# Optimization experiments

Measured on AMD Instinct MI355X. Metric: run time of the kernel, lower is better.

Reference implementation:

```python
import jax, jax.numpy as jnp
import numpy as np

K = 1024          # num_embeddings
D = 64            # embedding_dim
EPS = 0.05        # entropic regularization epsilon
DUAL_STEPS = 10
DUAL_LR = 0.5
TEMP = 0.5        # hist_temperature
OT_W = 1.0
CC = 0.25         # commitment cost


def _norm_prob(p):
    p = jnp.clip(p, 1e-12)
    return p / p.sum()


def _dual_obj(phi, src_w, tgt_w, cost):
    src_w = _norm_prob(src_w)
    tgt_w = _norm_prob(tgt_w)
    log_tgt = jnp.log(jnp.clip(tgt_w, 1e-12))[None, :]          # [1, K]
    lse = jax.scipy.special.logsumexp(log_tgt + (-cost + phi[None, :]) / EPS, axis=1)  # [K]
    return jnp.sum(src_w * (-EPS * lse)) + jnp.sum(tgt_w * phi)


def _dual_ot_loss(src_w, tgt_w, cost):
    src_d = jax.lax.stop_gradient(src_w)
    tgt_d = jax.lax.stop_gradient(tgt_w)
    cost_d = jax.lax.stop_gradient(cost)
    grad_phi = jax.grad(_dual_obj)
    def body(_, phi):
        return phi + DUAL_LR * grad_phi(phi, src_d, tgt_d, cost_d)
    phi = jax.lax.fori_loop(0, DUAL_STEPS, body, jnp.zeros_like(tgt_d))
    return _dual_obj(jax.lax.stop_gradient(phi), src_w, tgt_w, cost)


def _gaussian_target():
    idx = jnp.arange(K, dtype=jnp.float32)
    mean = (K - 1) / 2.0
    std = K / 6.0
    t = jnp.exp(-0.5 * ((idx - mean) / std) ** 2)
    return t / jnp.clip(t.sum(), 1e-12)


def _forward(inputs, codebook):
    B, C, H, W = inputs.shape
    x_bhwc = jnp.transpose(inputs, (0, 2, 3, 1))                 # [B,H,W,C]
    flat = x_bhwc.reshape(-1, C)                                  # [N, D]
    # squared-distance matrix [N, K]
    d = (jnp.sum(flat * flat, axis=1, keepdims=True)
         + jnp.sum(codebook * codebook, axis=1)
         - 2.0 * flat @ codebook.T)
    idx = jnp.argmin(d, axis=1)                                   # [N]
    enc = jax.nn.one_hot(idx, K, dtype=jnp.float32)               # [N, K]
    # power normalize (one-hot power = sqrt(1/K) < 1, so a no-op, but faithful)
    power = jnp.sqrt(jnp.mean(enc * enc))
    enc = jnp.where(power > 1.0, enc / power, enc)
    clean_q = enc @ codebook                                      # [N, D]
    noisy_q = clean_q                                             # channel=None -> zero noise
    # training losses
    hard_hist = jnp.mean(enc, axis=0)                             # [K]
    soft = jax.nn.softmax(-d / TEMP, axis=1)                      # [N, K]
    soft_hist = jnp.mean(soft, axis=0)
    # value = hard_hist, gradient flows via soft_hist (straight-through hist)
    cw = _norm_prob(hard_hist + soft_hist - jax.lax.stop_gradient(soft_hist))
    target = _gaussian_target()
    support = jnp.arange(K, dtype=jnp.float32)
    cost = jnp.abs(support[:, None] - support[None, :])           # cdist(p=2) on 1-d support
    ot_loss = OT_W * _dual_ot_loss(cw, target, cost)
    codebook_loss = jnp.mean((clean_q - jax.lax.stop_gradient(flat)) ** 2)
    commit_loss = jnp.mean((jax.lax.stop_gradient(clean_q) - flat) ** 2)
    loss = codebook_loss + CC * commit_loss + ot_loss
    # straight-through quantized output
    nq = noisy_q.reshape(B, H, W, C)
    quantized = x_bhwc + jax.lax.stop_gradient(nq - x_bhwc)
    quantized = jnp.transpose(quantized, (0, 3, 1, 2))            # [B,C,H,W]
    avg = jnp.mean(enc, axis=0)
    perplexity = jnp.exp(-jnp.sum(avg * jnp.log(avg + 1e-10)))
    return quantized, loss, perplexity


def setup_inputs() -> dict:
    key = jax.random.key(0)
    k1, k2 = jax.random.split(key)
    inputs = jax.random.normal(k1, (32, D, 32, 32), dtype=jnp.float32)
    codebook = jax.random.uniform(k2, (K, D), minval=-1.0 / K, maxval=1.0 / K, dtype=jnp.float32)
    return {"inputs": inputs, "codebook": codebook}


def reference(inputs, codebook):
    return _forward(inputs, codebook)
```

## Files before the change

kernel.cpp:

```cpp
#include <hip/hip_runtime.h>
#include <math.h>

#define NPTS 32768
#define KCB  1024
#define DIM  64
#define HW   1024
#define CHW  65536

typedef short  bf16x8 __attribute__((ext_vector_type(8)));
typedef float  f32x16 __attribute__((ext_vector_type(16)));

__device__ __forceinline__ unsigned short f2b_rne(float f) {
  unsigned u = __float_as_uint(f);
  unsigned r = 0x7FFFu + ((u >> 16) & 1u);
  return (unsigned short)((u + r) >> 16);
}

__device__ __forceinline__ float block_sum(float v, float* scratch) {
  #pragma unroll
  for (int o = 32; o > 0; o >>= 1) v += __shfl_down(v, o, 64);
  int wid  = threadIdx.x >> 6;
  int lane = threadIdx.x & 63;
  __syncthreads();
  if (lane == 0) scratch[wid] = v;
  __syncthreads();
  float s = 0.f;
  int nw = blockDim.x >> 6;
  for (int w = 0; w < nw; ++w) s += scratch[w];
  return s;
}

__global__ __launch_bounds__(64) void k_cvt(const float* __restrict__ cb,
                                            float4* __restrict__ cbf,
                                            float* __restrict__ cnorm,
                                            int* __restrict__ hist,
                                            int* __restrict__ done2) {
  int c = blockIdx.x * 64 + threadIdx.x;
  hist[c] = 0;
  if (c == 0) *done2 = 0;
  const float4* row4 = (const float4*)(cb + c * DIM);
  float4 r[16];
  #pragma unroll
  for (int i = 0; i < 16; ++i) r[i] = row4[i];
  float s = 0.f;
  #pragma unroll
  for (int i = 0; i < 16; ++i) {
    s = fmaf(r[i].x, r[i].x, s); s = fmaf(r[i].y, r[i].y, s);
    s = fmaf(r[i].z, r[i].z, s); s = fmaf(r[i].w, r[i].w, s);
  }
  cnorm[c] = s;
  int ch = c >> 6, nt = (c >> 5) & 1, n = c & 31;
  int base = ch * 512 + nt * 256 + n;
  #pragma unroll
  for (int o = 0; o < 8; ++o) {
    float f[8] = {r[2*o].x, r[2*o].y, r[2*o].z, r[2*o].w,
                  r[2*o+1].x, r[2*o+1].y, r[2*o+1].z, r[2*o+1].w};
    unsigned hu[4];
    #pragma unroll
    for (int j = 0; j < 4; ++j) {
      unsigned short h0 = f2b_rne(f[2*j]), h1 = f2b_rne(f[2*j+1]);
      hu[j] = (unsigned)h0 | ((unsigned)h1 << 16);
    }
    int pos = base + (o >> 1) * 64 + (o & 1) * 32;
    uint4 hv = {hu[0], hu[1], hu[2], hu[3]};
    cbf[pos] = *(float4*)&hv;
  }
}

__global__ __launch_bounds__(256, 2) void k_dist(const float* __restrict__ x,
                                                 const float* __restrict__ cb,
                                                 const float4* __restrict__ cbf,
                                                 const float* __restrict__ cnorm,
                                                 int* __restrict__ hist,
                                                 float* __restrict__ msep,
                                                 int* __restrict__ done2,
                                                 float* __restrict__ out) {
  __shared__ __align__(16) union SM {
    struct {
      unsigned short lph[64][72];
      float cn[KCB];
    } g;
    struct {
      float lt[KCB + 8]; float src[KCB + 8]; float phi[KCB + 8]; float lse[KCB + 8];
    } o;
  } sm;
  __shared__ float s_sx[64], s_part[4][64];
  __shared__ unsigned long long s_pk[64][2];
  __shared__ int   s_bd[64];
  __shared__ float scratch[4];
  __shared__ int   s_flag;

  int tid = threadIdx.x;
  int t   = blockIdx.x;
  int n0  = t * 64;
  int b   = n0 >> 10;
  int hw0 = n0 & 1023;

  *(float4*)&sm.g.cn[tid * 4] = *(const float4*)(cnorm + tid * 4);

  float fx[16];
  {
    int p = tid & 63, q4 = tid >> 6;
    const float* xb = x + b * CHW + hw0 + p;
    float s = 0.f;
    unsigned short hb[16];
    #pragma unroll
    for (int i = 0; i < 16; ++i) {
      int c = q4 * 16 + i;
      float f = xb[c * HW];
      fx[i] = f;
      s = fmaf(f, f, s);
      hb[i] = f2b_rne(f);
    }
    s_part[q4][p] = s;
    #pragma unroll
    for (int j = 0; j < 8; ++j)
      *(unsigned*)&sm.g.lph[p][q4 * 16 + 2 * j] =
          (unsigned)hb[2*j] | ((unsigned)hb[2*j+1] << 16);
  }
  __syncthreads();
  if (tid < 64)
    s_sx[tid] = ((s_part[0][tid] + s_part[1][tid]) + s_part[2][tid]) + s_part[3][tid];
  __syncthreads();

  int w = tid >> 6, l = tid & 63;
  int wm = w >> 1, wn = w & 1;
  int u = l >> 5, n = l & 31;

  bf16x8 ah[4];
  {
    int pt = wm * 32 + n;
    #pragma unroll
    for (int s = 0; s < 4; ++s)
      ah[s] = *(const bf16x8*)&sm.g.lph[pt][(2 * s + u) * 8];
  }
  float sxr[16];
  #pragma unroll
  for (int r = 0; r < 16; ++r)
    sxr[r] = s_sx[wm * 32 + (r & 3) + 8 * (r >> 2) + 4 * u];

  float best[16]; int bidx[16];
  #pragma unroll
  for (int r = 0; r < 16; ++r) { best[r] = 3.4e38f; bidx[r] = 0; }

  int bofs = wn * 256 + u * 32 + n;
  const bf16x8* gb = (const bf16x8*)cbf;

  bf16x8 cbh[4], nbh[4];
  #pragma unroll
  for (int s = 0; s < 4; ++s) cbh[s] = gb[bofs + s * 64];

  #pragma unroll
  for (int ch = 0; ch < 16; ++ch) {
    if (ch < 15) {
      const bf16x8* gn = gb + (ch + 1) * 512;
      #pragma unroll
      for (int s = 0; s < 4; ++s) nbh[s] = gn[bofs + s * 64];
    }
    f32x16 acc;
    #pragma unroll
    for (int r = 0; r < 16; ++r) acc[r] = 0.f;
    #pragma unroll
    for (int s = 0; s < 4; ++s)
      acc = __builtin_amdgcn_mfma_f32_32x32x16_bf16(ah[s], cbh[s], acc, 0, 0, 0);
    int   kk  = ch * 64 + wn * 32 + n;
    float cnv = sm.g.cn[kk];
    #pragma unroll
    for (int r = 0; r < 16; ++r) {
      float dist = (sxr[r] + cnv) - 2.0f * acc[r];
      if (dist < best[r]) { best[r] = dist; bidx[r] = kk; }
    }
    if (ch < 15) {
      #pragma unroll
      for (int s = 0; s < 4; ++s) cbh[s] = nbh[s];
    }
  }

  #pragma unroll
  for (int r = 0; r < 16; ++r) {
    unsigned long long p =
        ((unsigned long long)__float_as_uint(best[r]) << 32) | (unsigned)bidx[r];
    #pragma unroll
    for (int m = 1; m < 32; m <<= 1) {
      unsigned long long o = __shfl_xor(p, m, 64);
      p = (o < p) ? o : p;
    }
    if (n == 0)
      s_pk[wm * 32 + (r & 3) + 8 * (r >> 2) + 4 * u][wn] = p;
  }
  __syncthreads();
  if (tid < 64) {
    unsigned long long a = s_pk[tid][0], c2 = s_pk[tid][1];
    unsigned long long mn = (c2 < a) ? c2 : a;
    int bd = (int)(mn & 0xffffffffull);
    s_bd[tid] = bd;
    atomicAdd(&hist[bd], 1);
  }
  __syncthreads();

  float se = 0.f;
  {
    int p = tid & 63, cg2 = tid >> 6;
    int bd = s_bd[p];
    const float* crow = cb + bd * DIM;
    float* ob = out + b * CHW + hw0 + p;
    #pragma unroll 4
    for (int i = 0; i < 16; ++i) {
      int c = cg2 * 16 + i;
      float xv   = fx[i];
      float diff = crow[c] - xv;
      se += diff * diff;
      ob[c * HW] = xv + diff;
    }
  }
  float tot = block_sum(se, scratch);
  if (tid == 0) msep[t] = tot;

  __syncthreads();
  if (tid == 0) { __threadfence(); s_flag = atomicAdd(done2, 1); }
  __syncthreads();
  if (s_flag != 511) return;
  __threadfence();

  {
    int i0  = tid * 4;
    int sl0 = i0 + 4;

    float mse_a = __hip_atomic_load(&msep[tid],       __ATOMIC_RELAXED, __HIP_MEMORY_SCOPE_AGENT);
    float mse_b = __hip_atomic_load(&msep[tid + 256], __ATOMIC_RELAXED, __HIP_MEMORY_SCOPE_AGENT);
    float msetot = block_sum(mse_a + mse_b, scratch);

    int hi[4];
    #pragma unroll
    for (int j = 0; j < 4; ++j)
      hi[j] = __hip_atomic_load(&hist[i0 + j], __ATOMIC_RELAXED,
                                __HIP_MEMORY_SCOPE_AGENT);
    float tj[4], hj[4];
    #pragma unroll
    for (int j = 0; j < 4; ++j) {
      float fi = (float)(i0 + j);
      float zz = (fi - 511.5f) / (1024.0f / 6.0f);
      tj[j] = expf(-0.5f * zz * zz);
      hj[j] = (float)hi[j] * (1.0f / 32768.0f);
    }
    float St = block_sum(tj[0] + tj[1] + tj[2] + tj[3], scratch);
    float tgt[4], ltw[4];
    float l2 = 0.f;
    #pragma unroll
    for (int j = 0; j < 4; ++j) { tgt[j] = fmaxf(tj[j] / fmaxf(St, 1e-12f), 1e-12f); l2 += tgt[j]; }
    float St2 = block_sum(l2, scratch);
    #pragma unroll
    for (int j = 0; j < 4; ++j) { tgt[j] = tgt[j] / St2; ltw[j] = logf(fmaxf(tgt[j], 1e-12f)); }

    float m1[4], srcw[4];
    float l3 = 0.f;
    #pragma unroll
    for (int j = 0; j < 4; ++j) { m1[j] = fmaxf(hj[j], 1e-12f); l3 += m1[j]; }
    float S1 = block_sum(l3, scratch);
    float l4 = 0.f;
    #pragma unroll
    for (int j = 0; j < 4; ++j) { srcw[j] = fmaxf(m1[j] / S1, 1e-12f); l4 += srcw[j]; }
    float S2 = block_sum(l4, scratch);
    float l5 = 0.f;
    #pragma unroll
    for (int j = 0; j < 4; ++j) { srcw[j] = srcw[j] / S2; l5 += hj[j] * logf(hj[j] + 1e-10f); }
    float ent = block_sum(l5, scratch);

    *(float4*)&sm.o.lt[sl0]  = *(float4*)ltw;
    *(float4*)&sm.o.src[sl0] = *(float4*)srcw;
    *(float4*)&sm.o.phi[sl0] = make_float4(0.f, 0.f, 0.f, 0.f);
    *(float4*)&sm.o.lse[sl0] = make_float4(0.f, 0.f, 0.f, 0.f);
    if (tid == 0) {
      #pragma unroll
      for (int p = 0; p < 4; ++p) {
        sm.o.lt[p] = -100.f; sm.o.src[p] = 0.f; sm.o.phi[p] = 0.f; sm.o.lse[p] = 0.f;
        sm.o.lt[KCB+4+p] = -100.f; sm.o.src[KCB+4+p] = 0.f;
        sm.o.phi[KCB+4+p] = 0.f;   sm.o.lse[KCB+4+p] = 0.f;
      }
    }
    __syncthreads();

    float ws[12];
    #pragma unroll
    for (int m = 0; m < 3; ++m) *(float4*)&ws[m*4] = *(float4*)&sm.o.src[i0 + m*4];

    float phi[4] = {0.f, 0.f, 0.f, 0.f};
    float lse[4];
    for (int it = 0; it <= 10; ++it) {
      float wl[12], wp[12];
      #pragma unroll
      for (int m = 0; m < 3; ++m) {
        *(float4*)&wl[m*4] = *(float4*)&sm.o.lt[i0 + m*4];
        *(float4*)&wp[m*4] = *(float4*)&sm.o.phi[i0 + m*4];
      }
      #pragma unroll
      for (int j = 0; j < 4; ++j) {
        float mx = -3.0e38f;
        float vv[5];
        #pragma unroll
        for (int qq = 0; qq < 5; ++qq) {
          int m = j + qq + 2;
          float a = wl[m] + (wp[m] - fabsf((float)(qq - 2))) * 20.0f;
          vv[qq] = a;
          mx = fmaxf(mx, a);
        }
        float ssum = 0.f;
        #pragma unroll
        for (int qq = 0; qq < 5; ++qq) ssum += expf(vv[qq] - mx);
        lse[j] = mx + logf(ssum);
      }
      *(float4*)&sm.o.lse[sl0] = *(float4*)lse;
      __syncthreads();
      if (it == 10) break;

      float we[12];
      #pragma unroll
      for (int m = 0; m < 3; ++m) *(float4*)&we[m*4] = *(float4*)&sm.o.lse[i0 + m*4];
      #pragma unroll
      for (int j = 0; j < 4; ++j) {
        float basej = ltw[j] + phi[j] * 20.0f;
        float cs = 0.f;
        #pragma unroll
        for (int qq = 0; qq < 5; ++qq) {
          int m = j + qq + 2;
          float a = basej - fabsf((float)(qq - 2)) * 20.0f;
          cs += ws[m] * expf(a - we[m]);
        }
        phi[j] += 0.5f * (tgt[j] - cs);
      }
      *(float4*)&sm.o.phi[sl0] = *(float4*)phi;
      __syncthreads();
    }

    float lo = 0.f;
    #pragma unroll
    for (int j = 0; j < 4; ++j) lo += srcw[j] * (-0.05f * lse[j]) + tgt[j] * phi[j];
    float ot = block_sum(lo, scratch);

    if (tid == 0) {
      out[2097152] = 1.25f * (msetot * (1.0f / 2097152.0f)) + ot;
      out[2097153] = expf(-ent);
    }
  }
}

extern "C" void kernel_launch(void* const* d_in, const int* in_sizes, int n_in,
                              void* d_out, int out_size, void* d_ws, size_t ws_size,
                              hipStream_t stream) {
  const float* x  = (const float*)d_in[0];
  const float* cb = (const float*)d_in[1];
  float* out = (float*)d_out;

  float4* cbf  = (float4*)d_ws;
  float*  cnorm = (float*)((char*)d_ws + 131072);
  int*    hist  = (int*)((char*)d_ws + 135168);
  float*  msep  = (float*)((char*)d_ws + 139264);
  int*    done2 = (int*)((char*)d_ws + 141312);

  k_cvt<<<16, 64, 0, stream>>>(cb, cbf, cnorm, hist, done2);
  k_dist<<<512, 256, 0, stream>>>(x, cb, cbf, cnorm, hist, msep, done2, out);
}
```

Baseline: 118.0 us.

## Double block size and split codebook chunks across two wave halves

Launches k_dist with 512 threads per block instead of 256. Each half of the block scans half of the codebook chunks, and the partial argmins are merged through a wider shared array. Per-thread channel loads and stores are halved, and the final OT tail is gated to the first 256 threads. The aim is more waves in flight per point tile to hide latency on the codebook loads and MFMA work. In exchange it adds a larger cross-wave reduction and raises register and occupancy pressure under the new launch bounds.

```diff
diff --git a/kernel.cpp b/kernel.cpp
--- a/kernel.cpp
+++ b/kernel.cpp
@@ -67,7 +67,7 @@
   }
 }
 
-__global__ __launch_bounds__(256, 2) void k_dist(const float* __restrict__ x,
+__global__ __launch_bounds__(512, 2) void k_dist(const float* __restrict__ x,
                                                  const float* __restrict__ cb,
                                                  const float4* __restrict__ cbf,
                                                  const float* __restrict__ cnorm,
@@ -84,10 +84,10 @@
       float lt[KCB + 8]; float src[KCB + 8]; float phi[KCB + 8]; float lse[KCB + 8];
     } o;
   } sm;
-  __shared__ float s_sx[64], s_part[4][64];
-  __shared__ unsigned long long s_pk[64][2];
+  __shared__ float s_sx[64], s_part[8][64];
+  __shared__ unsigned long long s_pk[64][4];
   __shared__ int   s_bd[64];
-  __shared__ float scratch[4];
+  __shared__ float scratch[8];
   __shared__ int   s_flag;
 
   int tid = threadIdx.x;
@@ -96,35 +96,39 @@
   int b   = n0 >> 10;
   int hw0 = n0 & 1023;
 
-  *(float4*)&sm.g.cn[tid * 4] = *(const float4*)(cnorm + tid * 4);
-
-  float fx[16];
-  {
-    int p = tid & 63, q4 = tid >> 6;
+  *(float2*)&sm.g.cn[tid * 2] = *(const float2*)(cnorm + tid * 2);
+
+  float fx[8];
+  {
+    int p = tid & 63, q8 = tid >> 6;
     const float* xb = x + b * CHW + hw0 + p;
     float s = 0.f;
-    unsigned short hb[16];
-    #pragma unroll
-    for (int i = 0; i < 16; ++i) {
-      int c = q4 * 16 + i;
+    unsigned short hb[8];
+    #pragma unroll
+    for (int i = 0; i < 8; ++i) {
+      int c = q8 * 8 + i;
       float f = xb[c * HW];
       fx[i] = f;
       s = fmaf(f, f, s);
       hb[i] = f2b_rne(f);
     }
-    s_part[q4][p] = s;
-    #pragma unroll
-    for (int j = 0; j < 8; ++j)
-      *(unsigned*)&sm.g.lph[p][q4 * 16 + 2 * j] =
+    s_part[q8][p] = s;
+    #pragma unroll
+    for (int j = 0; j < 4; ++j)
+      *(unsigned*)&sm.g.lph[p][q8 * 8 + 2 * j] =
           (unsigned)hb[2*j] | ((unsigned)hb[2*j+1] << 16);
   }
   __syncthreads();
-  if (tid < 64)
-    s_sx[tid] = ((s_part[0][tid] + s_part[1][tid]) + s_part[2][tid]) + s_part[3][tid];
+  if (tid < 64) {
+    float s = s_part[0][tid];
+    #pragma unroll
+    for (int q = 1; q < 8; ++q) s += s_part[q][tid];
+    s_sx[tid] = s;
+  }
   __syncthreads();
 
   int w = tid >> 6, l = tid & 63;
-  int wm = w >> 1, wn = w & 1;
+  int h = w >> 2, wm = (w >> 1) & 1, wn = w & 1;
   int u = l >> 5, n = l & 31;
 
   bf16x8 ah[4];
@@ -147,13 +151,17 @@
   const bf16x8* gb = (const bf16x8*)cbf;
 
   bf16x8 cbh[4], nbh[4];
-  #pragma unroll
-  for (int s = 0; s < 4; ++s) cbh[s] = gb[bofs + s * 64];
-
-  #pragma unroll
-  for (int ch = 0; ch < 16; ++ch) {
-    if (ch < 15) {
-      const bf16x8* gn = gb + (ch + 1) * 512;
+  {
+    const bf16x8* g0 = gb + (h * 8) * 512;
+    #pragma unroll
+    for (int s = 0; s < 4; ++s) cbh[s] = g0[bofs + s * 64];
+  }
+
+  #pragma unroll
+  for (int i = 0; i < 8; ++i) {
+    int gc = h * 8 + i;
+    if (i < 7) {
+      const bf16x8* gn = gb + (gc + 1) * 512;
       #pragma unroll
       for (int s = 0; s < 4; ++s) nbh[s] = gn[bofs + s * 64];
     }
@@ -163,14 +171,14 @@
     #pragma unroll
     for (int s = 0; s < 4; ++s)
       acc = __builtin_amdgcn_mfma_f32_32x32x16_bf16(ah[s], cbh[s], acc, 0, 0, 0);
-    int   kk  = ch * 64 + wn * 32 + n;
+    int   kk  = gc * 64 + wn * 32 + n;
     float cnv = sm.g.cn[kk];
     #pragma unroll
     for (int r = 0; r < 16; ++r) {
       float dist = (sxr[r] + cnv) - 2.0f * acc[r];
       if (dist < best[r]) { best[r] = dist; bidx[r] = kk; }
     }
-    if (ch < 15) {
+    if (i < 7) {
       #pragma unroll
       for (int s = 0; s < 4; ++s) cbh[s] = nbh[s];
     }
@@ -186,11 +194,14 @@
       p = (o < p) ? o : p;
     }
     if (n == 0)
-      s_pk[wm * 32 + (r & 3) + 8 * (r >> 2) + 4 * u][wn] = p;
+      s_pk[wm * 32 + (r & 3) + 8 * (r >> 2) + 4 * u][h * 2 + wn] = p;
   }
   __syncthreads();
   if (tid < 64) {
-    unsigned long long a = s_pk[tid][0], c2 = s_pk[tid][1];
+    unsigned long long m0 = s_pk[tid][0], m1 = s_pk[tid][1];
+    unsigned long long m2 = s_pk[tid][2], m3 = s_pk[tid][3];
+    unsigned long long a  = (m1 < m0) ? m1 : m0;
+    unsigned long long c2 = (m3 < m2) ? m3 : m2;
     unsigned long long mn = (c2 < a) ? c2 : a;
     int bd = (int)(mn & 0xffffffffull);
     s_bd[tid] = bd;
@@ -204,9 +215,9 @@
     int bd = s_bd[p];
     const float* crow = cb + bd * DIM;
     float* ob = out + b * CHW + hw0 + p;
-    #pragma unroll 4
-    for (int i = 0; i < 16; ++i) {
-      int c = cg2 * 16 + i;
+    #pragma unroll
+    for (int i = 0; i < 8; ++i) {
+      int c = cg2 * 8 + i;
       float xv   = fx[i];
       float diff = crow[c] - xv;
       se += diff * diff;
@@ -226,50 +237,64 @@
     int i0  = tid * 4;
     int sl0 = i0 + 4;
 
-    float mse_a = __hip_atomic_load(&msep[tid],       __ATOMIC_RELAXED, __HIP_MEMORY_SCOPE_AGENT);
-    float mse_b = __hip_atomic_load(&msep[tid + 256], __ATOMIC_RELAXED, __HIP_MEMORY_SCOPE_AGENT);
-    float msetot = block_sum(mse_a + mse_b, scratch);
-
-    int hi[4];
-    #pragma unroll
-    for (int j = 0; j < 4; ++j)
-      hi[j] = __hip_atomic_load(&hist[i0 + j], __ATOMIC_RELAXED,
-                                __HIP_MEMORY_SCOPE_AGENT);
-    float tj[4], hj[4];
-    #pragma unroll
-    for (int j = 0; j < 4; ++j) {
-      float fi = (float)(i0 + j);
-      float zz = (fi - 511.5f) / (1024.0f / 6.0f);
-      tj[j] = expf(-0.5f * zz * zz);
-      hj[j] = (float)hi[j] * (1.0f / 32768.0f);
-    }
-    float St = block_sum(tj[0] + tj[1] + tj[2] + tj[3], scratch);
-    float tgt[4], ltw[4];
+    float msum = __hip_atomic_load(&msep[tid], __ATOMIC_RELAXED,
+                                   __HIP_MEMORY_SCOPE_AGENT);
+    float msetot = block_sum(msum, scratch);
+
+    float tj[4], hj[4], tgt[4], ltw[4], srcw[4];
+    float tsum = 0.f;
+    if (tid < 256) {
+      int hi[4];
+      #pragma unroll
+      for (int j = 0; j < 4; ++j)
+        hi[j] = __hip_atomic_load(&hist[i0 + j], __ATOMIC_RELAXED,
+                                  __HIP_MEMORY_SCOPE_AGENT);
+      #pragma unroll
+      for (int j = 0; j < 4; ++j) {
+        float fi = (float)(i0 + j);
+        float zz = (fi - 511.5f) / (1024.0f / 6.0f);
+        tj[j] = expf(-0.5f * zz * zz);
+        hj[j] = (float)hi[j] * (1.0f / 32768.0f);
+      }
+      tsum = tj[0] + tj[1] + tj[2] + tj[3];
+    }
+    float St = block_sum(tsum, scratch);
     float l2 = 0.f;
-    #pragma unroll
-    for (int j = 0; j < 4; ++j) { tgt[j] = fmaxf(tj[j] / fmaxf(St, 1e-12f), 1e-12f); l2 += tgt[j]; }
+    if (tid < 256) {
+      #pragma unroll
+      for (int j = 0; j < 4; ++j) { tgt[j] = fmaxf(tj[j] / fmaxf(St, 1e-12f), 1e-12f); l2 += tgt[j]; }
+    }
     float St2 = block_sum(l2, scratch);
-    #pragma unroll
-    for (int j = 0; j < 4; ++j) { tgt[j] = tgt[j] / St2; ltw[j] = logf(fmaxf(tgt[j], 1e-12f)); }
-
-    float m1[4], srcw[4];
+    if (tid < 256) {
+      #pragma unroll
+      for (int j = 0; j < 4; ++j) { tgt[j] = tgt[j] / St2; ltw[j] = logf(fmaxf(tgt[j], 1e-12f)); }
+    }
+    float m1[4];
     float l3 = 0.f;
-    #pragma unroll
-    for (int j = 0; j < 4; ++j) { m1[j] = fmaxf(hj[j], 1e-12f); l3 += m1[j]; }
+    if (tid < 256) {
+      #pragma unroll
+      for (int j = 0; j < 4; ++j) { m1[j] = fmaxf(hj[j], 1e-12f); l3 += m1[j]; }
+    }
     float S1 = block_sum(l3, scratch);
     float l4 = 0.f;
-    #pragma unroll
-    for (int j = 0; j < 4; ++j) { srcw[j] = fmaxf(m1[j] / S1, 1e-12f); l4 += srcw[j]; }
+    if (tid < 256) {
+      #pragma unroll
+      for (int j = 0; j < 4; ++j) { srcw[j] = fmaxf(m1[j] / S1, 1e-12f); l4 += srcw[j]; }
+    }
     float S2 = block_sum(l4, scratch);
     float l5 = 0.f;
-    #pragma unroll
-    for (int j = 0; j < 4; ++j) { srcw[j] = srcw[j] / S2; l5 += hj[j] * logf(hj[j] + 1e-10f); }
+    if (tid < 256) {
+      #pragma unroll
+      for (int j = 0; j < 4; ++j) { srcw[j] = srcw[j] / S2; l5 += hj[j] * logf(hj[j] + 1e-10f); }
+    }
     float ent = block_sum(l5, scratch);
 
-    *(float4*)&sm.o.lt[sl0]  = *(float4*)ltw;
-    *(float4*)&sm.o.src[sl0] = *(float4*)srcw;
-    *(float4*)&sm.o.phi[sl0] = make_float4(0.f, 0.f, 0.f, 0.f);
-    *(float4*)&sm.o.lse[sl0] = make_float4(0.f, 0.f, 0.f, 0.f);
+    if (tid < 256) {
+      *(float4*)&sm.o.lt[sl0]  = *(float4*)ltw;
+      *(float4*)&sm.o.src[sl0] = *(float4*)srcw;
+      *(float4*)&sm.o.phi[sl0] = make_float4(0.f, 0.f, 0.f, 0.f);
+      *(float4*)&sm.o.lse[sl0] = make_float4(0.f, 0.f, 0.f, 0.f);
+    }
     if (tid == 0) {
       #pragma unroll
       for (int p = 0; p < 4; ++p) {
@@ -281,60 +306,68 @@
     __syncthreads();
 
     float ws[12];
-    #pragma unroll
-    for (int m = 0; m < 3; ++m) *(float4*)&ws[m*4] = *(float4*)&sm.o.src[i0 + m*4];
+    if (tid < 256) {
+      #pragma unroll
+      for (int m = 0; m < 3; ++m) *(float4*)&ws[m*4] = *(float4*)&sm.o.src[i0 + m*4];
+    }
 
     float phi[4] = {0.f, 0.f, 0.f, 0.f};
     float lse[4];
     for (int it = 0; it <= 10; ++it) {
-      float wl[12], wp[12];
-      #pragma unroll
-      for (int m = 0; m < 3; ++m) {
-        *(float4*)&wl[m*4] = *(float4*)&sm.o.lt[i0 + m*4];
-        *(float4*)&wp[m*4] = *(float4*)&sm.o.phi[i0 + m*4];
+      if (tid < 256) {
+        float wl[12], wp[12];
+        #pragma unroll
+        for (int m = 0; m < 3; ++m) {
+          *(float4*)&wl[m*4] = *(float4*)&sm.o.lt[i0 + m*4];
+          *(float4*)&wp[m*4] = *(float4*)&sm.o.phi[i0 + m*4];
+        }
+        #pragma unroll
+        for (int j = 0; j < 4; ++j) {
+          float mx = -3.0e38f;
+          float vv[5];
+          #pragma unroll
+          for (int qq = 0; qq < 5; ++qq) {
+            int m = j + qq + 2;
+            float a = wl[m] + (wp[m] - fabsf((float)(qq - 2))) * 20.0f;
+            vv[qq] = a;
+            mx = fmaxf(mx, a);
+          }
+          float ssum = 0.f;
+          #pragma unroll
+          for (int qq = 0; qq < 5; ++qq) ssum += expf(vv[qq] - mx);
+          lse[j] = mx + logf(ssum);
+        }
+        *(float4*)&sm.o.lse[sl0] = *(float4*)lse;
       }
-      #pragma unroll
-      for (int j = 0; j < 4; ++j) {
-        float mx = -3.0e38f;
-        float vv[5];
-        #pragma unroll
-        for (int qq = 0; qq < 5; ++qq) {
-          int m = j + qq + 2;
-          float a = wl[m] + (wp[m] - fabsf((float)(qq - 2))) * 20.0f;
-          vv[qq] = a;
-          mx = fmaxf(mx, a);
-        }
-        float ssum = 0.f;
-        #pragma unroll
-        for (int qq = 0; qq < 5; ++qq) ssum += expf(vv[qq] - mx);
-        lse[j] = mx + logf(ssum);
-      }
-      *(float4*)&sm.o.lse[sl0] = *(float4*)lse;
       __syncthreads();
       if (it == 10) break;
 
-      float we[12];
-      #pragma unroll
-      for (int m = 0; m < 3; ++m) *(float4*)&we[m*4] = *(float4*)&sm.o.lse[i0 + m*4];
-      #pragma unroll
-      for (int j = 0; j < 4; ++j) {
-        float basej = ltw[j] + phi[j] * 20.0f;
-        float cs = 0.f;
+      if (tid < 256) {
+        float we[12];
         #pragma unroll
-        for (int qq = 0; qq < 5; ++qq) {
-          int m = j + qq + 2;
-          float a = basej - fabsf((float)(qq - 2)) * 20.0f;
-          cs += ws[m] * expf(a - we[m]);
+        for (int m = 0; m < 3; ++m) *(float4*)&we[m*4] = *(float4*)&sm.o.lse[i0 + m*4];
+        #pragma unroll
+        for (int j = 0; j < 4; ++j) {
+          float basej = ltw[j] + phi[j] * 20.0f;
+          float cs = 0.f;
+          #pragma unroll
+          for (int qq = 0; qq < 5; ++qq) {
+            int m = j + qq + 2;
+            float a = basej - fabsf((float)(qq - 2)) * 20.0f;
+            cs += ws[m] * expf(a - we[m]);
+          }
+          phi[j] += 0.5f * (tgt[j] - cs);
         }
-        phi[j] += 0.5f * (tgt[j] - cs);
+        *(float4*)&sm.o.phi[sl0] = *(float4*)phi;
       }
-      *(float4*)&sm.o.phi[sl0] = *(float4*)phi;
       __syncthreads();
     }
 
     float lo = 0.f;
-    #pragma unroll
-    for (int j = 0; j < 4; ++j) lo += srcw[j] * (-0.05f * lse[j]) + tgt[j] * phi[j];
+    if (tid < 256) {
+      #pragma unroll
+      for (int j = 0; j < 4; ++j) lo += srcw[j] * (-0.05f * lse[j]) + tgt[j] * phi[j];
+    }
     float ot = block_sum(lo, scratch);
 
     if (tid == 0) {
@@ -358,5 +391,5 @@
   int*    done2 = (int*)((char*)d_ws + 141312);
 
   k_cvt<<<16, 64, 0, stream>>>(cb, cbf, cnorm, hist, done2);
-  k_dist<<<512, 256, 0, stream>>>(x, cb, cbf, cnorm, hist, msep, done2, out);
-}
+  k_dist<<<512, 512, 0, stream>>>(x, cb, cbf, cnorm, hist, msep, done2, out);
+}
```

Result: slower. 125.7 us (+6.5%).
